# Kernel optimization log

Measured on AMD Instinct MI355X. Metric: run time of the kernel, lower is better.

The kernel has to match this reference:

```python
import jax, jax.numpy as jnp
import numpy as np

N, CAT_IN, H, V, T = 256, 1024, 512, 32000, 8


def setup_inputs() -> dict:
    key = jax.random.key(0)
    ks = jax.random.split(key, 9)
    s = 0.05
    return {
        "context": jax.random.normal(ks[0], (N, CAT_IN), jnp.float32),
        "W_merge": jax.random.normal(ks[1], (H, CAT_IN), jnp.float32) * s,
        "b_merge": jax.random.normal(ks[2], (H,), jnp.float32) * s,
        "W_ih": jax.random.normal(ks[3], (4 * H, H), jnp.float32) * s,
        "W_hh": jax.random.normal(ks[4], (4 * H, H), jnp.float32) * s,
        "b_ih": jax.random.normal(ks[5], (4 * H,), jnp.float32) * s,
        "b_hh": jax.random.normal(ks[6], (4 * H,), jnp.float32) * s,
        "W_out": jax.random.normal(ks[7], (V, H), jnp.float32) * s,
        "b_out": jax.random.normal(ks[8], (V,), jnp.float32) * s,
        "max_subtoken_len": T,
    }


def reference(context, W_merge, b_merge, W_ih, W_hh, b_ih, b_hh, W_out, b_out, max_subtoken_len):
    # merge_func_g_emb: [N, CAT_IN] -> [N, H]
    ctx = context @ W_merge.T + b_merge
    # input projection is constant across steps (same context fed every step)
    x_proj = ctx @ W_ih.T + b_ih  # [N, 4H]
    hdim = W_hh.shape[1]

    def step(carry, _):
        h, c = carry
        gates = x_proj + h @ W_hh.T + b_hh  # [N, 4H]
        i, f, g, o = jnp.split(gates, 4, axis=-1)  # PyTorch LSTM gate order i,f,g,o
        i = jax.nn.sigmoid(i)
        f = jax.nn.sigmoid(f)
        g = jnp.tanh(g)
        o = jax.nn.sigmoid(o)
        c = f * c + i * g
        h = o * jnp.tanh(c)
        logits = h @ W_out.T + b_out  # [N, V]
        return (h, c), logits

    h0 = jnp.zeros((context.shape[0], hdim), context.dtype)
    c0 = jnp.zeros_like(h0)
    _, logits = jax.lax.scan(step, (h0, c0), None, length=max_subtoken_len)  # [T, N, V]
    return jnp.transpose(logits, (1, 0, 2))  # [N, T, V]
```

## Files before the change

kernel.cpp:

```cpp
#include <hip/hip_runtime.h>


#define GLOBAL_AS __attribute__((address_space(1)))
#define LDS_AS __attribute__((address_space(3)))

typedef __attribute__((ext_vector_type(8))) short short8;
typedef __attribute__((ext_vector_type(4))) float f32x4;

constexpr int N_  = 256;
constexpr int CIN = 1024;
constexpr int H_  = 512;
constexpr int G4  = 2048;
constexpr int V_  = 32000;
constexpr int T_  = 8;

__device__ inline short f2bf(float f) {
  union { float f; unsigned u; } v; v.f = f;
  unsigned r = v.u + 0x7fffu + ((v.u >> 16) & 1u);
  return (short)(r >> 16);
}

__device__ inline void async16(const void* g, void* l) {
  __builtin_amdgcn_global_load_lds((const GLOBAL_AS unsigned*)g,
                                   (LDS_AS unsigned*)l, 16, 0, 0);
}

__device__ inline float sigm(float x) { return 1.0f / (1.0f + __expf(-x)); }
__device__ inline float tanh_fast(float x) {
  x = fminf(15.0f, fmaxf(-15.0f, x));
  float e = __expf(2.0f * x);
  return (e - 1.0f) / (e + 1.0f);
}

__global__ __launch_bounds__(256) void cvt_bf16_4(const float* __restrict__ in,
                                                  short* __restrict__ out, int n4) {
  int i = blockIdx.x * 256 + threadIdx.x;
  if (i >= n4) return;
  float4 v = ((const float4*)in)[i];
  short4 s;
  s.x = f2bf(v.x); s.y = f2bf(v.y); s.z = f2bf(v.z); s.w = f2bf(v.w);
  ((short4*)out)[i] = s;
}

__global__ __launch_bounds__(256) void cvt_multi(
    const float* __restrict__ s0, short* __restrict__ d0, int c0,
    const float* __restrict__ s1, short* __restrict__ d1, int c1,
    const float* __restrict__ s2, short* __restrict__ d2, int c2,
    const float* __restrict__ s3, short* __restrict__ d3, int c3) {
  int i = blockIdx.x * 256 + threadIdx.x;
  const float* s; short* d; int k;
  if (i < c0)                { s = s0; d = d0; k = i; }
  else if (i < c0 + c1)      { s = s1; d = d1; k = i - c0; }
  else if (i < c0 + c1 + c2) { s = s2; d = d2; k = i - c0 - c1; }
  else if (i < c0 + c1 + c2 + c3) { s = s3; d = d3; k = i - c0 - c1 - c2; }
  else return;
  float4 v = ((const float4*)s)[k];
  short4 o;
  o.x = f2bf(v.x); o.y = f2bf(v.y); o.z = f2bf(v.z); o.w = f2bf(v.w);
  ((short4*)d)[k] = o;
}

template<int BM, int BN, int MODE>
__global__ __launch_bounds__(256) void gemm_bf16_bt(
    const short* __restrict__ A, const short* __restrict__ B,
    const float* __restrict__ bias1, const float* __restrict__ bias2,
    void* __restrict__ Cv, int M, int N, int K)
{
  constexpr int RT = BM / 32;
  constexpr int CT = BN / 32;
  __shared__ short As[BM * 32];
  __shared__ short Bs[BN * 32];

  const int tid = threadIdx.x;
  const int lane = tid & 63;
  const int w = tid >> 6;
  const int wr = w >> 1, wc = w & 1;
  const int m0 = blockIdx.y * BM;
  const int n0 = blockIdx.x * BN;
  const int rlane = lane & 15;
  const int klane = (lane >> 4) * 8;

  f32x4 acc[RT][CT] = {};

  for (int kc = 0; kc < K; kc += 32) {
#pragma unroll
    for (int it = 0; it < (BM * 4) / 256; ++it) {
      int idx = it * 256 + tid;
      const short* g = A + (size_t)(m0 + (idx >> 2)) * K + kc + (idx & 3) * 8;
      async16(g, &As[(size_t)(it * 256 + (tid & ~63)) * 8]);
    }
#pragma unroll
    for (int it = 0; it < (BN * 4) / 256; ++it) {
      int idx = it * 256 + tid;
      const short* g = B + (size_t)(n0 + (idx >> 2)) * K + kc + (idx & 3) * 8;
      async16(g, &Bs[(size_t)(it * 256 + (tid & ~63)) * 8]);
    }
    __syncthreads();

    short8 af[RT], bf[CT];
#pragma unroll
    for (int rt = 0; rt < RT; ++rt)
      af[rt] = *(const short8*)&As[(wr * (RT * 16) + rt * 16 + rlane) * 32 + klane];
#pragma unroll
    for (int ct = 0; ct < CT; ++ct)
      bf[ct] = *(const short8*)&Bs[(wc * (CT * 16) + ct * 16 + rlane) * 32 + klane];
#pragma unroll
    for (int rt = 0; rt < RT; ++rt)
#pragma unroll
      for (int ct = 0; ct < CT; ++ct)
        acc[rt][ct] = __builtin_amdgcn_mfma_f32_16x16x32_bf16(af[rt], bf[ct],
                                                              acc[rt][ct], 0, 0, 0);
    __syncthreads();
  }

#pragma unroll
  for (int ct = 0; ct < CT; ++ct) {
    int ng = n0 + wc * (CT * 16) + ct * 16 + rlane;
    float bv = (bias1 ? bias1[ng] : 0.0f) + (bias2 ? bias2[ng] : 0.0f);
#pragma unroll
    for (int rt = 0; rt < RT; ++rt)
#pragma unroll
      for (int r = 0; r < 4; ++r) {
        int mg = m0 + wr * (RT * 16) + rt * 16 + (lane >> 4) * 4 + r;
        float v = acc[rt][ct][r] + bv;
        if (MODE == 2) {
          int t = mg >> 8, nb = mg & 255;
          ((float*)Cv)[(size_t)nb * (T_ * V_) + (size_t)t * V_ + ng] = v;
        } else if (MODE == 1) {
          ((short*)Cv)[(size_t)mg * N + ng] = f2bf(v);
        } else {
          ((float*)Cv)[(size_t)mg * N + ng] = v;
        }
      }
  }
}

__global__ __launch_bounds__(256) void lstm_step(
    const short* __restrict__ Hprev,
    const short* __restrict__ Whh,
    const float* __restrict__ X,
    float* __restrict__ c,
    short* __restrict__ Hnext,
    int first)
{
  __shared__ char lds_raw[16384];
  short* As = (short*)lds_raw;
  short* Bs = (short*)(lds_raw + 4096);
  float* G  = (float*)lds_raw;

  const int tid = threadIdx.x;
  const int lane = tid & 63;
  const int w = tid >> 6;
  const int j0 = blockIdx.x * 32;
  const int n0 = blockIdx.y * 32;
  const int rlane = lane & 15;
  const int klane = (lane >> 4) * 8;
  const int qrow = (lane >> 4) * 4;

  f32x4 acc[2][2];
#pragma unroll
  for (int rt = 0; rt < 2; ++rt)
#pragma unroll
    for (int ct = 0; ct < 2; ++ct)
#pragma unroll
      for (int r = 0; r < 4; ++r)
        acc[rt][ct][r] = X[(size_t)(n0 + rt * 16 + qrow + r) * G4
                           + w * H_ + j0 + ct * 16 + rlane];

  if (!first) {
    for (int kc = 0; kc < H_; kc += 32) {
      if (w < 2)
        async16(Hprev + (size_t)(n0 + (tid >> 2)) * H_ + kc + (tid & 3) * 8,
                &As[(size_t)(tid & ~63) * 8]);
#pragma unroll
      for (int p = 0; p < 2; ++p) {
        int idx = p * 256 + tid;
        int br = idx >> 2, q = idx & 3;
        int g = br >> 5, jj = br & 31;
        async16(Whh + (size_t)(g * H_ + j0 + jj) * H_ + kc + q * 8,
                &Bs[(size_t)(idx & ~63) * 8]);
      }
      __syncthreads();
      short8 a0 = *(const short8*)&As[(0 * 16 + rlane) * 32 + klane];
      short8 a1 = *(const short8*)&As[(1 * 16 + rlane) * 32 + klane];
      short8 b0 = *(const short8*)&Bs[(w * 32 + 0 * 16 + rlane) * 32 + klane];
      short8 b1 = *(const short8*)&Bs[(w * 32 + 1 * 16 + rlane) * 32 + klane];
      acc[0][0] = __builtin_amdgcn_mfma_f32_16x16x32_bf16(a0, b0, acc[0][0], 0, 0, 0);
      acc[0][1] = __builtin_amdgcn_mfma_f32_16x16x32_bf16(a0, b1, acc[0][1], 0, 0, 0);
      acc[1][0] = __builtin_amdgcn_mfma_f32_16x16x32_bf16(a1, b0, acc[1][0], 0, 0, 0);
      acc[1][1] = __builtin_amdgcn_mfma_f32_16x16x32_bf16(a1, b1, acc[1][1], 0, 0, 0);
      __syncthreads();
    }
  }

#pragma unroll
  for (int rt = 0; rt < 2; ++rt)
#pragma unroll
    for (int ct = 0; ct < 2; ++ct)
#pragma unroll
      for (int r = 0; r < 4; ++r)
        G[(size_t)(w * 32 + rt * 16 + qrow + r) * 32 + ct * 16 + rlane] =
            acc[rt][ct][r];
  __syncthreads();

  int n = tid >> 3, jq = tid & 7;
  float4 gi = ((const float4*)G)[(0 * 32 + n) * 8 + jq];
  float4 gf = ((const float4*)G)[(1 * 32 + n) * 8 + jq];
  float4 gg = ((const float4*)G)[(2 * 32 + n) * 8 + jq];
  float4 go = ((const float4*)G)[(3 * 32 + n) * 8 + jq];
  size_t cix = (size_t)(n0 + n) * H_ + j0 + jq * 4;
  float4 cold = make_float4(0.f, 0.f, 0.f, 0.f);
  if (!first) cold = *(const float4*)&c[cix];
  float ci[4] = {gi.x, gi.y, gi.z, gi.w};
  float cf[4] = {gf.x, gf.y, gf.z, gf.w};
  float cg[4] = {gg.x, gg.y, gg.z, gg.w};
  float co[4] = {go.x, go.y, go.z, go.w};
  float cc[4] = {cold.x, cold.y, cold.z, cold.w};
  float4 cnew; short4 hnew;
  float* cn = &cnew.x;
  short hv[4];
#pragma unroll
  for (int e = 0; e < 4; ++e) {
    float ii = sigm(ci[e]), ff = sigm(cf[e]), g2 = tanh_fast(cg[e]), oo = sigm(co[e]);
    float cval = ff * cc[e] + ii * g2;
    cn[e] = cval;
    hv[e] = f2bf(oo * tanh_fast(cval));
  }
  hnew.x = hv[0]; hnew.y = hv[1]; hnew.z = hv[2]; hnew.w = hv[3];
  *(float4*)&c[cix] = cnew;
  *(short4*)&Hnext[cix] = hnew;
}

extern "C" void kernel_launch(void* const* d_in, const int* in_sizes, int n_in,
                              void* d_out, int out_size, void* d_ws, size_t ws_size,
                              hipStream_t stream)
{
  (void)in_sizes; (void)n_in; (void)out_size; (void)ws_size;
  const float* context = (const float*)d_in[0];
  const float* W_merge = (const float*)d_in[1];
  const float* b_merge = (const float*)d_in[2];
  const float* W_ih    = (const float*)d_in[3];
  const float* W_hh    = (const float*)d_in[4];
  const float* b_ih    = (const float*)d_in[5];
  const float* b_hh    = (const float*)d_in[6];
  const float* W_out   = (const float*)d_in[7];
  const float* b_out   = (const float*)d_in[8];
  float* out = (float*)d_out;

  char* p = (char*)d_ws;
  short* Wout_b = (short*)p;  p += (size_t)V_ * H_ * 2;
  short* Whh_b  = (short*)p;  p += (size_t)G4 * H_ * 2;
  short* Wih_b  = (short*)p;  p += (size_t)G4 * H_ * 2;
  short* Wmrg_b = (short*)p;  p += (size_t)H_ * CIN * 2;
  short* Ctxin_b= (short*)p;  p += (size_t)N_ * CIN * 2;
  short* Ctx_b  = (short*)p;  p += (size_t)N_ * H_ * 2;
  short* Hall   = (short*)p;  p += (size_t)T_ * N_ * H_ * 2;
  float* X      = (float*)p;  p += (size_t)N_ * G4 * 4;
  float* c      = (float*)p;  p += (size_t)N_ * H_ * 4;

  cvt_bf16_4<<<(V_ * H_ / 4 + 255) / 256, 256, 0, stream>>>(W_out, Wout_b, V_ * H_ / 4);
  {
    int c0 = N_ * CIN / 4, c1 = H_ * CIN / 4, c2 = G4 * H_ / 4, c3 = G4 * H_ / 4;
    int tot = c0 + c1 + c2 + c3;
    cvt_multi<<<(tot + 255) / 256, 256, 0, stream>>>(
        context, Ctxin_b, c0, W_merge, Wmrg_b, c1,
        W_ih, Wih_b, c2, W_hh, Whh_b, c3);
  }

  gemm_bf16_bt<64, 64, 1><<<dim3(H_ / 64, N_ / 64), 256, 0, stream>>>(
      Ctxin_b, Wmrg_b, b_merge, nullptr, Ctx_b, N_, H_, CIN);
  gemm_bf16_bt<64, 64, 0><<<dim3(G4 / 64, N_ / 64), 256, 0, stream>>>(
      Ctx_b, Wih_b, b_ih, b_hh, X, N_, G4, H_);

  for (int t = 0; t < T_; ++t) {
    const short* hp = (t == 0) ? Hall : Hall + (size_t)(t - 1) * N_ * H_;
    lstm_step<<<dim3(H_ / 32, N_ / 32), 256, 0, stream>>>(
        hp, Whh_b, X, c, Hall + (size_t)t * N_ * H_, t == 0 ? 1 : 0);
  }

  gemm_bf16_bt<128, 128, 2><<<dim3(V_ / 128, (T_ * N_) / 128), 256, 0, stream>>>(
      Hall, Wout_b, b_out, nullptr, out, T_ * N_, V_, H_);
}
```

Measured before the change: 537.1 us.

## Fuse merge GEMM, input projection and LSTM recurrence into one persistent kernel

Merges the context merge GEMM, the input projection and all eight LSTM steps into a single persistent kernel of 128 blocks. The blocks synchronise through per-row-group atomic grid barriers, keep W_hh slices resident in swizzled LDS, and hold the cell state and x-projection in registers. This removes about ten kernel launches, the global X and c buffers, and the repeated W_hh reloads, and also folds the two conversion kernels into one. The cost is spin barriers that assume all blocks are co-resident, plus a large LDS footprint that limits the kernel to one block per CU.

```diff
diff --git a/kernel.cpp b/kernel.cpp
--- a/kernel.cpp
+++ b/kernel.cpp
@@ -32,32 +32,225 @@
   return (e - 1.0f) / (e + 1.0f);
 }
 
-__global__ __launch_bounds__(256) void cvt_bf16_4(const float* __restrict__ in,
-                                                  short* __restrict__ out, int n4) {
-  int i = blockIdx.x * 256 + threadIdx.x;
-  if (i >= n4) return;
-  float4 v = ((const float4*)in)[i];
-  short4 s;
-  s.x = f2bf(v.x); s.y = f2bf(v.y); s.z = f2bf(v.z); s.w = f2bf(v.w);
-  ((short4*)out)[i] = s;
-}
-
-__global__ __launch_bounds__(256) void cvt_multi(
+__device__ inline void gbar(unsigned* cnt) {
+  __threadfence();
+  __syncthreads();
+  if (threadIdx.x == 0) {
+    unsigned v = atomicAdd(cnt, 1u);
+    unsigned tgt = (v & ~15u) + 16u;
+    while (atomicAdd(cnt, 0u) < tgt) __builtin_amdgcn_s_sleep(2);
+  }
+  __syncthreads();
+  __threadfence();
+}
+
+__global__ __launch_bounds__(256) void cvt_all(
     const float* __restrict__ s0, short* __restrict__ d0, int c0,
     const float* __restrict__ s1, short* __restrict__ d1, int c1,
     const float* __restrict__ s2, short* __restrict__ d2, int c2,
-    const float* __restrict__ s3, short* __restrict__ d3, int c3) {
+    const float* __restrict__ s3, short* __restrict__ d3, int c3,
+    const float* __restrict__ s4, short* __restrict__ d4, int c4,
+    unsigned* __restrict__ bar) {
   int i = blockIdx.x * 256 + threadIdx.x;
+  if (blockIdx.x == 0) bar[threadIdx.x] = 0u;
   const float* s; short* d; int k;
-  if (i < c0)                { s = s0; d = d0; k = i; }
-  else if (i < c0 + c1)      { s = s1; d = d1; k = i - c0; }
-  else if (i < c0 + c1 + c2) { s = s2; d = d2; k = i - c0 - c1; }
-  else if (i < c0 + c1 + c2 + c3) { s = s3; d = d3; k = i - c0 - c1 - c2; }
+  if (i < c0)                          { s = s0; d = d0; k = i; }
+  else if (i < c0 + c1)                { s = s1; d = d1; k = i - c0; }
+  else if (i < c0 + c1 + c2)           { s = s2; d = d2; k = i - c0 - c1; }
+  else if (i < c0 + c1 + c2 + c3)      { s = s3; d = d3; k = i - c0 - c1 - c2; }
+  else if (i < c0 + c1 + c2 + c3 + c4) { s = s4; d = d4; k = i - c0 - c1 - c2 - c3; }
   else return;
   float4 v = ((const float4*)s)[k];
   short4 o;
   o.x = f2bf(v.x); o.y = f2bf(v.y); o.z = f2bf(v.z); o.w = f2bf(v.w);
   ((short4*)d)[k] = o;
+}
+
+__global__ __launch_bounds__(256, 1) void decoder_core(
+    const short* __restrict__ Ctxin,
+    const short* __restrict__ Wmrg,
+    const float* __restrict__ bmrg,
+    const short* __restrict__ Wih,
+    const short* __restrict__ Whh,
+    const float* __restrict__ bih,
+    const float* __restrict__ bhh,
+    short* __restrict__ ctx,
+    short* __restrict__ Hall,
+    unsigned* __restrict__ bar)
+{
+  __shared__ alignas(16) short WhhL[128 * H_];
+  __shared__ alignas(16) char scratch[32768];
+
+  const int tid   = threadIdx.x;
+  const int lane  = tid & 63;
+  const int w     = tid >> 6;
+  const int rlane = lane & 15;
+  const int klane = (lane >> 4) * 8;
+  const int qrow  = (lane >> 4) * 4;
+  const int j0    = blockIdx.x * 32;
+  const int n0    = blockIdx.y * 32;
+  unsigned* mybar = bar + blockIdx.y * 32;
+  const int swz   = (rlane & 7) << 4;
+
+#pragma unroll
+  for (int i = 0; i < 32; ++i) {
+    int c = i * 256 + tid;
+    int r = c >> 6, cq = c & 63;
+    int ks = ((cq << 4) ^ ((r & 7) << 4)) >> 1;
+    async16(Whh + (size_t)((r >> 5) * H_ + j0 + (r & 31)) * H_ + ks,
+            &WhhL[(size_t)(i * 256 + (tid & ~63)) * 8]);
+  }
+
+  {
+    short* Aw = (short*)scratch + w * 2048;
+    short* Bw = Aw + 1024;
+    f32x4 m00 = {0,0,0,0}, m01 = {0,0,0,0}, m10 = {0,0,0,0}, m11 = {0,0,0,0};
+    const int kb = w * 256;
+    for (int i = 0; i < 8; ++i) {
+      int kc = kb + i * 32;
+#pragma unroll
+      for (int p = 0; p < 2; ++p) {
+        int cA = p * 64 + lane;
+        async16(Ctxin + (size_t)(n0 + (cA >> 2)) * CIN + kc + (cA & 3) * 8,
+                Aw + p * 512);
+        async16(Wmrg + (size_t)(j0 + (cA >> 2)) * CIN + kc + (cA & 3) * 8,
+                Bw + p * 512);
+      }
+      asm volatile("s_waitcnt vmcnt(0)" ::: "memory");
+      __builtin_amdgcn_sched_barrier(0);
+      short8 ma0 = *(const short8*)&Aw[rlane * 32 + klane];
+      short8 ma1 = *(const short8*)&Aw[(16 + rlane) * 32 + klane];
+      short8 mb0 = *(const short8*)&Bw[rlane * 32 + klane];
+      short8 mb1 = *(const short8*)&Bw[(16 + rlane) * 32 + klane];
+      m00 = __builtin_amdgcn_mfma_f32_16x16x32_bf16(ma0, mb0, m00, 0, 0, 0);
+      m01 = __builtin_amdgcn_mfma_f32_16x16x32_bf16(ma0, mb1, m01, 0, 0, 0);
+      m10 = __builtin_amdgcn_mfma_f32_16x16x32_bf16(ma1, mb0, m10, 0, 0, 0);
+      m11 = __builtin_amdgcn_mfma_f32_16x16x32_bf16(ma1, mb1, m11, 0, 0, 0);
+      asm volatile("s_waitcnt lgkmcnt(0)" ::: "memory");
+      __builtin_amdgcn_sched_barrier(0);
+    }
+    __syncthreads();
+    float* G = (float*)scratch;
+#pragma unroll
+    for (int r = 0; r < 4; ++r) {
+      G[(w * 32 + qrow + r) * 32 + rlane]           = m00[r];
+      G[(w * 32 + qrow + r) * 32 + 16 + rlane]      = m01[r];
+      G[(w * 32 + 16 + qrow + r) * 32 + rlane]      = m10[r];
+      G[(w * 32 + 16 + qrow + r) * 32 + 16 + rlane] = m11[r];
+    }
+    __syncthreads();
+    int nn = tid >> 3, jq = tid & 7;
+    const float4* Gv = (const float4*)scratch;
+    float4 p0 = Gv[(0 * 32 + nn) * 8 + jq];
+    float4 p1 = Gv[(1 * 32 + nn) * 8 + jq];
+    float4 p2 = Gv[(2 * 32 + nn) * 8 + jq];
+    float4 p3 = Gv[(3 * 32 + nn) * 8 + jq];
+    int jb = j0 + jq * 4;
+    short4 o;
+    o.x = f2bf(p0.x + p1.x + p2.x + p3.x + bmrg[jb + 0]);
+    o.y = f2bf(p0.y + p1.y + p2.y + p3.y + bmrg[jb + 1]);
+    o.z = f2bf(p0.z + p1.z + p2.z + p3.z + bmrg[jb + 2]);
+    o.w = f2bf(p0.w + p1.w + p2.w + p3.w + bmrg[jb + 3]);
+    *(short4*)&ctx[(size_t)(n0 + nn) * H_ + jb] = o;
+  }
+  gbar(mybar);
+
+  f32x4 x00, x01, x10, x11;
+  {
+    int ng0 = w * H_ + j0 + rlane, ng1 = ng0 + 16;
+    float bc0 = bih[ng0] + bhh[ng0];
+    float bc1 = bih[ng1] + bhh[ng1];
+    x00 = (f32x4){bc0, bc0, bc0, bc0};  x01 = (f32x4){bc1, bc1, bc1, bc1};
+    x10 = x00;                          x11 = x01;
+    short* As = (short*)scratch;
+    short* Bs = (short*)(scratch + 4096);
+    for (int kc = 0; kc < H_; kc += 32) {
+      if (w < 2)
+        async16(ctx + (size_t)(n0 + (tid >> 2)) * H_ + kc + (tid & 3) * 8,
+                &As[(tid & ~63) * 8]);
+#pragma unroll
+      for (int p = 0; p < 2; ++p) {
+        int idx = p * 256 + tid;
+        int br = idx >> 2, q = idx & 3;
+        async16(Wih + (size_t)((br >> 5) * H_ + j0 + (br & 31)) * H_ + q * 8 + kc,
+                &Bs[(idx & ~63) * 8]);
+      }
+      __syncthreads();
+      short8 xa0 = *(const short8*)&As[rlane * 32 + klane];
+      short8 xa1 = *(const short8*)&As[(16 + rlane) * 32 + klane];
+      short8 xb0 = *(const short8*)&Bs[(w * 32 + rlane) * 32 + klane];
+      short8 xb1 = *(const short8*)&Bs[(w * 32 + 16 + rlane) * 32 + klane];
+      x00 = __builtin_amdgcn_mfma_f32_16x16x32_bf16(xa0, xb0, x00, 0, 0, 0);
+      x01 = __builtin_amdgcn_mfma_f32_16x16x32_bf16(xa0, xb1, x01, 0, 0, 0);
+      x10 = __builtin_amdgcn_mfma_f32_16x16x32_bf16(xa1, xb0, x10, 0, 0, 0);
+      x11 = __builtin_amdgcn_mfma_f32_16x16x32_bf16(xa1, xb1, x11, 0, 0, 0);
+      __syncthreads();
+    }
+  }
+
+  float creg[4] = {0.f, 0.f, 0.f, 0.f};
+  const int ne = tid >> 3, jq = tid & 7;
+  const int r_b0 = w * 32 + rlane, r_b1 = r_b0 + 16;
+  const char* WLb = (const char*)WhhL;
+  const char* HLb = (const char*)scratch;
+
+  for (int t = 0; t < T_; ++t) {
+    f32x4 a00 = x00, a01 = x01, a10 = x10, a11 = x11;
+    if (t > 0) {
+      const short* Hp = Hall + (size_t)(t - 1) * N_ * H_;
+#pragma unroll
+      for (int i = 0; i < 8; ++i) {
+        int c = i * 256 + tid;
+        int r = c >> 6, cq = c & 63;
+        int ks = ((cq << 4) ^ ((r & 7) << 4)) >> 1;
+        async16(Hp + (size_t)(n0 + r) * H_ + ks,
+                (void*)(HLb + (size_t)(i * 256 + (tid & ~63)) * 16));
+      }
+      __syncthreads();
+#pragma unroll
+      for (int kc = 0; kc < H_; kc += 32) {
+        int ko = (kc + klane) * 2;
+        short8 a0 = *(const short8*)(HLb + ((rlane * 1024 + ko) ^ swz));
+        short8 a1 = *(const short8*)(HLb + (((16 + rlane) * 1024 + ko) ^ swz));
+        short8 b0 = *(const short8*)(WLb + ((r_b0 * 1024 + ko) ^ swz));
+        short8 b1 = *(const short8*)(WLb + ((r_b1 * 1024 + ko) ^ swz));
+        a00 = __builtin_amdgcn_mfma_f32_16x16x32_bf16(a0, b0, a00, 0, 0, 0);
+        a01 = __builtin_amdgcn_mfma_f32_16x16x32_bf16(a0, b1, a01, 0, 0, 0);
+        a10 = __builtin_amdgcn_mfma_f32_16x16x32_bf16(a1, b0, a10, 0, 0, 0);
+        a11 = __builtin_amdgcn_mfma_f32_16x16x32_bf16(a1, b1, a11, 0, 0, 0);
+      }
+      __syncthreads();
+    }
+    float* G = (float*)scratch;
+#pragma unroll
+    for (int r = 0; r < 4; ++r) {
+      G[(w * 32 + qrow + r) * 32 + rlane]           = a00[r];
+      G[(w * 32 + qrow + r) * 32 + 16 + rlane]      = a01[r];
+      G[(w * 32 + 16 + qrow + r) * 32 + rlane]      = a10[r];
+      G[(w * 32 + 16 + qrow + r) * 32 + 16 + rlane] = a11[r];
+    }
+    __syncthreads();
+    float4 gi = ((const float4*)G)[(0 * 32 + ne) * 8 + jq];
+    float4 gf = ((const float4*)G)[(1 * 32 + ne) * 8 + jq];
+    float4 gg = ((const float4*)G)[(2 * 32 + ne) * 8 + jq];
+    float4 go = ((const float4*)G)[(3 * 32 + ne) * 8 + jq];
+    float pi[4] = {gi.x, gi.y, gi.z, gi.w};
+    float pf[4] = {gf.x, gf.y, gf.z, gf.w};
+    float pg[4] = {gg.x, gg.y, gg.z, gg.w};
+    float po[4] = {go.x, go.y, go.z, go.w};
+    short hv[4];
+#pragma unroll
+    for (int e = 0; e < 4; ++e) {
+      float ii = sigm(pi[e]), ff = sigm(pf[e]);
+      float g2 = tanh_fast(pg[e]), oo = sigm(po[e]);
+      float cv = ff * creg[e] + ii * g2;
+      creg[e] = cv;
+      hv[e] = f2bf(oo * tanh_fast(cv));
+    }
+    short4 h4; h4.x = hv[0]; h4.y = hv[1]; h4.z = hv[2]; h4.w = hv[3];
+    *(short4*)&Hall[(size_t)t * N_ * H_ + (size_t)(n0 + ne) * H_ + j0 + jq * 4] = h4;
+    if (t < T_ - 1) gbar(mybar);
+  }
 }
 
 template<int BM, int BN, int MODE>
@@ -133,102 +326,6 @@
         }
       }
   }
-}
-
-__global__ __launch_bounds__(256) void lstm_step(
-    const short* __restrict__ Hprev,
-    const short* __restrict__ Whh,
-    const float* __restrict__ X,
-    float* __restrict__ c,
-    short* __restrict__ Hnext,
-    int first)
-{
-  __shared__ char lds_raw[16384];
-  short* As = (short*)lds_raw;
-  short* Bs = (short*)(lds_raw + 4096);
-  float* G  = (float*)lds_raw;
-
-  const int tid = threadIdx.x;
-  const int lane = tid & 63;
-  const int w = tid >> 6;
-  const int j0 = blockIdx.x * 32;
-  const int n0 = blockIdx.y * 32;
-  const int rlane = lane & 15;
-  const int klane = (lane >> 4) * 8;
-  const int qrow = (lane >> 4) * 4;
-
-  f32x4 acc[2][2];
-#pragma unroll
-  for (int rt = 0; rt < 2; ++rt)
-#pragma unroll
-    for (int ct = 0; ct < 2; ++ct)
-#pragma unroll
-      for (int r = 0; r < 4; ++r)
-        acc[rt][ct][r] = X[(size_t)(n0 + rt * 16 + qrow + r) * G4
-                           + w * H_ + j0 + ct * 16 + rlane];
-
-  if (!first) {
-    for (int kc = 0; kc < H_; kc += 32) {
-      if (w < 2)
-        async16(Hprev + (size_t)(n0 + (tid >> 2)) * H_ + kc + (tid & 3) * 8,
-                &As[(size_t)(tid & ~63) * 8]);
-#pragma unroll
-      for (int p = 0; p < 2; ++p) {
-        int idx = p * 256 + tid;
-        int br = idx >> 2, q = idx & 3;
-        int g = br >> 5, jj = br & 31;
-        async16(Whh + (size_t)(g * H_ + j0 + jj) * H_ + kc + q * 8,
-                &Bs[(size_t)(idx & ~63) * 8]);
-      }
-      __syncthreads();
-      short8 a0 = *(const short8*)&As[(0 * 16 + rlane) * 32 + klane];
-      short8 a1 = *(const short8*)&As[(1 * 16 + rlane) * 32 + klane];
-      short8 b0 = *(const short8*)&Bs[(w * 32 + 0 * 16 + rlane) * 32 + klane];
-      short8 b1 = *(const short8*)&Bs[(w * 32 + 1 * 16 + rlane) * 32 + klane];
-      acc[0][0] = __builtin_amdgcn_mfma_f32_16x16x32_bf16(a0, b0, acc[0][0], 0, 0, 0);
-      acc[0][1] = __builtin_amdgcn_mfma_f32_16x16x32_bf16(a0, b1, acc[0][1], 0, 0, 0);
-      acc[1][0] = __builtin_amdgcn_mfma_f32_16x16x32_bf16(a1, b0, acc[1][0], 0, 0, 0);
-      acc[1][1] = __builtin_amdgcn_mfma_f32_16x16x32_bf16(a1, b1, acc[1][1], 0, 0, 0);
-      __syncthreads();
-    }
-  }
-
-#pragma unroll
-  for (int rt = 0; rt < 2; ++rt)
-#pragma unroll
-    for (int ct = 0; ct < 2; ++ct)
-#pragma unroll
-      for (int r = 0; r < 4; ++r)
-        G[(size_t)(w * 32 + rt * 16 + qrow + r) * 32 + ct * 16 + rlane] =
-            acc[rt][ct][r];
-  __syncthreads();
-
-  int n = tid >> 3, jq = tid & 7;
-  float4 gi = ((const float4*)G)[(0 * 32 + n) * 8 + jq];
-  float4 gf = ((const float4*)G)[(1 * 32 + n) * 8 + jq];
-  float4 gg = ((const float4*)G)[(2 * 32 + n) * 8 + jq];
-  float4 go = ((const float4*)G)[(3 * 32 + n) * 8 + jq];
-  size_t cix = (size_t)(n0 + n) * H_ + j0 + jq * 4;
-  float4 cold = make_float4(0.f, 0.f, 0.f, 0.f);
-  if (!first) cold = *(const float4*)&c[cix];
-  float ci[4] = {gi.x, gi.y, gi.z, gi.w};
-  float cf[4] = {gf.x, gf.y, gf.z, gf.w};
-  float cg[4] = {gg.x, gg.y, gg.z, gg.w};
-  float co[4] = {go.x, go.y, go.z, go.w};
-  float cc[4] = {cold.x, cold.y, cold.z, cold.w};
-  float4 cnew; short4 hnew;
-  float* cn = &cnew.x;
-  short hv[4];
-#pragma unroll
-  for (int e = 0; e < 4; ++e) {
-    float ii = sigm(ci[e]), ff = sigm(cf[e]), g2 = tanh_fast(cg[e]), oo = sigm(co[e]);
-    float cval = ff * cc[e] + ii * g2;
-    cn[e] = cval;
-    hv[e] = f2bf(oo * tanh_fast(cval));
-  }
-  hnew.x = hv[0]; hnew.y = hv[1]; hnew.z = hv[2]; hnew.w = hv[3];
-  *(float4*)&c[cix] = cnew;
-  *(short4*)&Hnext[cix] = hnew;
 }
 
 extern "C" void kernel_launch(void* const* d_in, const int* in_sizes, int n_in,
@@ -248,35 +345,26 @@
   float* out = (float*)d_out;
 
   char* p = (char*)d_ws;
-  short* Wout_b = (short*)p;  p += (size_t)V_ * H_ * 2;
-  short* Whh_b  = (short*)p;  p += (size_t)G4 * H_ * 2;
-  short* Wih_b  = (short*)p;  p += (size_t)G4 * H_ * 2;
-  short* Wmrg_b = (short*)p;  p += (size_t)H_ * CIN * 2;
-  short* Ctxin_b= (short*)p;  p += (size_t)N_ * CIN * 2;
-  short* Ctx_b  = (short*)p;  p += (size_t)N_ * H_ * 2;
-  short* Hall   = (short*)p;  p += (size_t)T_ * N_ * H_ * 2;
-  float* X      = (float*)p;  p += (size_t)N_ * G4 * 4;
-  float* c      = (float*)p;  p += (size_t)N_ * H_ * 4;
-
-  cvt_bf16_4<<<(V_ * H_ / 4 + 255) / 256, 256, 0, stream>>>(W_out, Wout_b, V_ * H_ / 4);
+  short* Wout_b  = (short*)p;  p += (size_t)V_ * H_ * 2;
+  short* Whh_b   = (short*)p;  p += (size_t)G4 * H_ * 2;
+  short* Wih_b   = (short*)p;  p += (size_t)G4 * H_ * 2;
+  short* Wmrg_b  = (short*)p;  p += (size_t)H_ * CIN * 2;
+  short* Ctxin_b = (short*)p;  p += (size_t)N_ * CIN * 2;
+  short* Ctx_b   = (short*)p;  p += (size_t)N_ * H_ * 2;
+  short* Hall    = (short*)p;  p += (size_t)T_ * N_ * H_ * 2;
+  unsigned* bar  = (unsigned*)p; p += 256 * 4;
+
   {
-    int c0 = N_ * CIN / 4, c1 = H_ * CIN / 4, c2 = G4 * H_ / 4, c3 = G4 * H_ / 4;
-    int tot = c0 + c1 + c2 + c3;
-    cvt_multi<<<(tot + 255) / 256, 256, 0, stream>>>(
-        context, Ctxin_b, c0, W_merge, Wmrg_b, c1,
-        W_ih, Wih_b, c2, W_hh, Whh_b, c3);
-  }
-
-  gemm_bf16_bt<64, 64, 1><<<dim3(H_ / 64, N_ / 64), 256, 0, stream>>>(
-      Ctxin_b, Wmrg_b, b_merge, nullptr, Ctx_b, N_, H_, CIN);
-  gemm_bf16_bt<64, 64, 0><<<dim3(G4 / 64, N_ / 64), 256, 0, stream>>>(
-      Ctx_b, Wih_b, b_ih, b_hh, X, N_, G4, H_);
-
-  for (int t = 0; t < T_; ++t) {
-    const short* hp = (t == 0) ? Hall : Hall + (size_t)(t - 1) * N_ * H_;
-    lstm_step<<<dim3(H_ / 32, N_ / 32), 256, 0, stream>>>(
-        hp, Whh_b, X, c, Hall + (size_t)t * N_ * H_, t == 0 ? 1 : 0);
-  }
+    int c0 = V_ * H_ / 4, c1 = N_ * CIN / 4, c2 = H_ * CIN / 4;
+    int c3 = G4 * H_ / 4, c4 = G4 * H_ / 4;
+    int tot = c0 + c1 + c2 + c3 + c4;
+    cvt_all<<<(tot + 255) / 256, 256, 0, stream>>>(
+        W_out, Wout_b, c0, context, Ctxin_b, c1, W_merge, Wmrg_b, c2,
+        W_ih, Wih_b, c3, W_hh, Whh_b, c4, bar);
+  }
+
+  decoder_core<<<dim3(H_ / 32, N_ / 32), 256, 0, stream>>>(
+      Ctxin_b, Wmrg_b, b_merge, Wih_b, Whh_b, b_ih, b_hh, Ctx_b, Hall, bar);
 
   gemm_bf16_bt<128, 128, 2><<<dim3(V_ / 128, (T_ * N_) / 128), 256, 0, stream>>>(
       Hall, Wout_b, b_out, nullptr, out, T_ * N_, V_, H_);
```

Result: slower. 616.7 us (+14.8%).
